# Performance work log

Hardware: AMD Instinct MI355X
Metric: run time of the kernel (lower is better)

The kernel has to match this reference:

```python
import jax, jax.numpy as jnp
import numpy as np

N_NODES = 50000
N_EDGES = 800000
N_GRAPHS = 8
BN_EPS = 1e-5


def setup_inputs() -> dict:
    key = jax.random.key(0)
    ks = iter(jax.random.split(key, 40))
    d = {}
    d["x"] = jax.random.normal(next(ks), (N_NODES, 3), dtype=jnp.float32)
    d["edge_index"] = jax.random.randint(next(ks), (2, N_EDGES), 0, N_NODES, dtype=jnp.int32)
    d["batch"] = jnp.sort(jax.random.randint(next(ks), (N_NODES,), 0, N_GRAPHS, dtype=jnp.int32))
    conv_in = [3, 64, 128]  # dense concat widths feeding each GCN layer
    for i, cin in enumerate(conv_in):
        d[f"W{i}"] = jax.random.normal(next(ks), (cin, 64), dtype=jnp.float32) * (1.0 / np.sqrt(cin))
        d[f"b{i}"] = jax.random.normal(next(ks), (64,), dtype=jnp.float32) * 0.05
        d[f"g{i}"] = jax.random.uniform(next(ks), (64,), dtype=jnp.float32) + 0.5
        d[f"beta{i}"] = jax.random.normal(next(ks), (64,), dtype=jnp.float32) * 0.05
        d[f"rm{i}"] = jax.random.normal(next(ks), (64,), dtype=jnp.float32) * 0.05
        d[f"rv{i}"] = jax.random.uniform(next(ks), (64,), dtype=jnp.float32) + 0.5
    def lin(k, i, o):
        return (jax.random.normal(k, (i, o), dtype=jnp.float32) * (1.0 / np.sqrt(i)),)
    d["enc_w0"], = lin(next(ks), 256, 128); d["enc_b0"] = jax.random.normal(next(ks), (128,), jnp.float32) * 0.05
    d["enc_w1"], = lin(next(ks), 128, 64); d["enc_b1"] = jax.random.normal(next(ks), (64,), jnp.float32) * 0.05
    d["dec_w0"], = lin(next(ks), 64, 32); d["dec_b0"] = jax.random.normal(next(ks), (32,), jnp.float32) * 0.05
    d["dec_w1"], = lin(next(ks), 32, 1); d["dec_b1"] = jax.random.normal(next(ks), (1,), jnp.float32) * 0.05
    return d


def reference(x, edge_index, batch,
              W0, b0, g0, beta0, rm0, rv0,
              W1, b1, g1, beta1, rm1, rv1,
              W2, b2, g2, beta2, rm2, rv2,
              enc_w0, enc_b0, enc_w1, enc_b1,
              dec_w0, dec_b0, dec_w1, dec_b1):
    N = x.shape[0]
    loops = jnp.arange(N, dtype=edge_index.dtype)
    src = jnp.concatenate([edge_index[0], loops])  # GCNConv adds self loops
    dst = jnp.concatenate([edge_index[1], loops])
    deg = jax.ops.segment_sum(jnp.ones_like(src, dtype=x.dtype), dst, num_segments=N)
    dinv = jnp.where(deg > 0, jax.lax.rsqrt(deg), 0.0)
    coef = (dinv[src] * dinv[dst])[:, None]  # symmetric normalization per edge

    def conv_bn_relu(h, W, b, g, beta, rm, rv):
        hw = h @ W                                    # [N, 64]
        out = jax.ops.segment_sum(hw[src] * coef, dst, num_segments=N) + b
        out = (out - rm) * (g * jax.lax.rsqrt(rv + BN_EPS)) + beta  # BN eval mode
        return jax.nn.relu(out)

    params = [(W0, b0, g0, beta0, rm0, rv0),
              (W1, b1, g1, beta1, rm1, rv1),
              (W2, b2, g2, beta2, rm2, rv2)]
    prev = []
    h = x
    for p in params:  # dense connectivity: concat all previous concat-outputs
        h = conv_bn_relu(h, *p)
        h = jnp.concatenate(prev + [h], axis=1)
        prev.append(h)

    e = jax.nn.relu(jax.nn.relu(h @ enc_w0 + enc_b0) @ enc_w1 + enc_b1)  # [N, 64]
    counts = jax.ops.segment_sum(jnp.ones((N,), x.dtype), batch, num_segments=N_GRAPHS)
    gfeat = jax.ops.segment_sum(e, batch, num_segments=N_GRAPHS) / jnp.maximum(counts, 1.0)[:, None]
    out = jax.nn.relu(gfeat @ dec_w0 + dec_b0) @ dec_w1 + dec_b1  # [G, 1]
    return out[:, 0]  # torch.squeeze(output, 1) since num_classes == 1
```

## Files before the change

kernel.cpp:

```cpp
#include <hip/hip_runtime.h>

#define NN 50000
#define NE 800000
#define NG 8
#define BN_EPS 1e-5f
#define NBLK ((NN + 255) / 256)
#define POOL_BLOCKS 512
#define NPART 8

typedef __attribute__((ext_vector_type(8))) short bf16x8;
typedef __attribute__((ext_vector_type(4))) float f32x4;

static __device__ __forceinline__ unsigned short f2bf(float f) {
    unsigned int u = __float_as_uint(f);
    unsigned int r = (u + 0x7FFFu + ((u >> 16) & 1u)) >> 16;
    return (unsigned short)r;
}
static __device__ __forceinline__ float bf2f(unsigned short h) {
    return __uint_as_float((unsigned int)h << 16);
}


__global__ __launch_bounds__(256) void count_deg(const int* __restrict__ dst,
                                                 int* __restrict__ degi) {
    int e = blockIdx.x * 256 + threadIdx.x;
    if (e < NE) atomicAdd(&degi[dst[e]], 1);
}

__global__ __launch_bounds__(256) void compute_dinv_xs(const int* __restrict__ degi,
                                                       const float* __restrict__ x,
                                                       float* __restrict__ dinv,
                                                       float* __restrict__ xs) {
    int i = blockIdx.x * 256 + threadIdx.x;
    if (i < NN) {
        float di = rsqrtf((float)(degi[i] + 1));
        dinv[i] = di;
        xs[i * 3 + 0] = x[i * 3 + 0] * di;
        xs[i * 3 + 1] = x[i * 3 + 1] * di;
        xs[i * 3 + 2] = x[i * 3 + 2] * di;
    }
}

__global__ __launch_bounds__(256) void scan_partial(const int* __restrict__ degi,
                                                    int* __restrict__ rowptr,
                                                    int* __restrict__ bsum) {
    __shared__ int sh[256];
    const int tid = threadIdx.x;
    const int i = blockIdx.x * 256 + tid;
    int v = (i < NN) ? degi[i] : 0;
    sh[tid] = v;
    __syncthreads();
#pragma unroll
    for (int off = 1; off < 256; off <<= 1) {
        int t = (tid >= off) ? sh[tid - off] : 0;
        __syncthreads();
        sh[tid] += t;
        __syncthreads();
    }
    if (i < NN) rowptr[i] = sh[tid] - v;
    if (tid == 255) bsum[blockIdx.x] = sh[255];
}

__global__ __launch_bounds__(256) void scan_bsums(int* __restrict__ bsum) {
    __shared__ int sh[256];
    const int tid = threadIdx.x;
    int v = (tid < NBLK) ? bsum[tid] : 0;
    sh[tid] = v;
    __syncthreads();
#pragma unroll
    for (int off = 1; off < 256; off <<= 1) {
        int t = (tid >= off) ? sh[tid - off] : 0;
        __syncthreads();
        sh[tid] += t;
        __syncthreads();
    }
    if (tid < NBLK) bsum[tid] = sh[tid] - v;
}

__global__ __launch_bounds__(256) void scan_finalize(const int* __restrict__ bsum,
                                                     int* __restrict__ rowptr,
                                                     int* __restrict__ cursor) {
    const int i = blockIdx.x * 256 + threadIdx.x;
    if (i < NN) {
        int r = rowptr[i] + bsum[blockIdx.x];
        rowptr[i] = r;
        cursor[i] = r;
    }
    if (i == 0) rowptr[NN] = NE;
}

__global__ __launch_bounds__(256) void fill_csr(const int* __restrict__ src,
                                                const int* __restrict__ dst,
                                                int* __restrict__ cursor,
                                                unsigned short* __restrict__ esrc16) {
    int e = blockIdx.x * 256 + threadIdx.x;
    if (e < NE) {
        int s = src[e], d = dst[e];
        int p = atomicAdd(&cursor[d], 1);
        esrc16[p] = (unsigned short)s;
    }
}


__global__ __launch_bounds__(256) void pack_w(const float* __restrict__ W, int K, int NOUT,
                                              unsigned short* __restrict__ ph,
                                              unsigned short* __restrict__ pl) {
    int idx = blockIdx.x * 256 + threadIdx.x;
    if (idx >= K * NOUT) return;
    int j = idx & 7;
    int lane = (idx >> 3) & 63;
    int rest = idx >> 9;
    int NF = NOUT >> 4;
    int f = rest % NF, ks = rest / NF;
    int k = ks * 32 + (lane >> 4) * 8 + j;
    int col = f * 16 + (lane & 15);
    float v = W[k * NOUT + col];
    unsigned short hi = f2bf(v);
    ph[idx] = hi;
    pl[idx] = f2bf(v - bf2f(hi));
}


template<int K, int NF, int MODE>
__global__ __launch_bounds__(256) void mfma_gemm(
        const unsigned short* __restrict__ Ahi,
        const unsigned short* __restrict__ Alo, int lda,
        const unsigned short* __restrict__ Bph,
        const unsigned short* __restrict__ Bpl,
        const float* __restrict__ bias,
        const float* __restrict__ dinv,
        float* __restrict__ outF,
        unsigned short* __restrict__ outHi,
        unsigned short* __restrict__ outLo, int ldo) {
    const int wave = threadIdx.x >> 6;
    const int lane = threadIdx.x & 63;
    const int rbase = blockIdx.x * 64 + wave * 16;
    int arow = rbase + (lane & 15);
    if (arow >= NN) arow = NN - 1;
    const int kbase = (lane >> 4) * 8;

    f32x4 acc[NF];
#pragma unroll
    for (int f = 0; f < NF; f++) acc[f] = (f32x4){0.f, 0.f, 0.f, 0.f};

    const unsigned short* pa_hi = Ahi + (size_t)arow * lda + kbase;
    const unsigned short* pa_lo = Alo + (size_t)arow * lda + kbase;
    const unsigned short* pb_hi = Bph + lane * 8;
    const unsigned short* pb_lo = Bpl + lane * 8;

#pragma unroll
    for (int ks = 0; ks < K / 32; ks++) {
        bf16x8 ah = *reinterpret_cast<const bf16x8*>(pa_hi + ks * 32);
        bf16x8 al = *reinterpret_cast<const bf16x8*>(pa_lo + ks * 32);
#pragma unroll
        for (int f = 0; f < NF; f++) {
            bf16x8 bh = *reinterpret_cast<const bf16x8*>(pb_hi + (size_t)((ks * NF + f) * 64) * 8);
            bf16x8 bl = *reinterpret_cast<const bf16x8*>(pb_lo + (size_t)((ks * NF + f) * 64) * 8);
            acc[f] = __builtin_amdgcn_mfma_f32_16x16x32_bf16(ah, bh, acc[f], 0, 0, 0);
            acc[f] = __builtin_amdgcn_mfma_f32_16x16x32_bf16(ah, bl, acc[f], 0, 0, 0);
            acc[f] = __builtin_amdgcn_mfma_f32_16x16x32_bf16(al, bh, acc[f], 0, 0, 0);
        }
    }

    const int drow0 = rbase + (lane >> 4) * 4;
    const int dcol = lane & 15;
#pragma unroll
    for (int f = 0; f < NF; f++) {
#pragma unroll
        for (int r = 0; r < 4; r++) {
            int row = drow0 + r;
            if (row < NN) {
                int col = f * 16 + dcol;
                float v = acc[f][r];
                if (MODE == 0) {
                    outF[(size_t)row * ldo + col] = v * dinv[row];
                } else {
                    v = fmaxf(v + bias[col], 0.0f);
                    if (MODE == 1) {
                        unsigned short hi = f2bf(v);
                        outHi[(size_t)row * ldo + col] = hi;
                        outLo[(size_t)row * ldo + col] = f2bf(v - bf2f(hi));
                    } else {
                        outF[(size_t)row * ldo + col] = v;
                    }
                }
            }
        }
    }
}


__global__ __launch_bounds__(256) void agg_x3(
        const float* __restrict__ xs,
        const int* __restrict__ rowptr,
        const unsigned short* __restrict__ esrc16,
        const float* __restrict__ dinv,
        float* __restrict__ ax) {
    const int i = blockIdx.x * 256 + threadIdx.x;
    if (i >= NN) return;
    float a0 = xs[i * 3 + 0];
    float a1 = xs[i * 3 + 1];
    float a2 = xs[i * 3 + 2];
    const int beg = rowptr[i], end = rowptr[i + 1];
    int e = beg;
    for (; e + 3 < end; e += 4) {
        int s0 = esrc16[e], s1 = esrc16[e + 1], s2 = esrc16[e + 2], s3 = esrc16[e + 3];
        a0 += xs[s0 * 3 + 0] + xs[s1 * 3 + 0] + xs[s2 * 3 + 0] + xs[s3 * 3 + 0];
        a1 += xs[s0 * 3 + 1] + xs[s1 * 3 + 1] + xs[s2 * 3 + 1] + xs[s3 * 3 + 1];
        a2 += xs[s0 * 3 + 2] + xs[s1 * 3 + 2] + xs[s2 * 3 + 2] + xs[s3 * 3 + 2];
    }
    for (; e < end; e++) {
        int s = esrc16[e];
        a0 += xs[s * 3 + 0];
        a1 += xs[s * 3 + 1];
        a2 += xs[s * 3 + 2];
    }
    const float di = dinv[i];
    ax[i * 3 + 0] = a0 * di;
    ax[i * 3 + 1] = a1 * di;
    ax[i * 3 + 2] = a2 * di;
}


__global__ __launch_bounds__(256) void l0_bn_relu(
        const float* __restrict__ ax, const float* __restrict__ W0,
        const float* __restrict__ b, const float* __restrict__ g,
        const float* __restrict__ beta, const float* __restrict__ rm,
        const float* __restrict__ rv,
        unsigned short* __restrict__ Hhi, unsigned short* __restrict__ Hlo) {
    const int t = blockIdx.x * 256 + threadIdx.x;
    const int row = t >> 6;
    const int ch = t & 63;
    if (row >= NN) return;
    float a0 = ax[row * 3 + 0], a1 = ax[row * 3 + 1], a2 = ax[row * 3 + 2];
    float v = a0 * W0[0 * 64 + ch] + a1 * W0[1 * 64 + ch] + a2 * W0[2 * 64 + ch] + b[ch];
    float sc = g[ch] * rsqrtf(rv[ch] + BN_EPS);
    v = (v - rm[ch]) * sc + beta[ch];
    v = fmaxf(v, 0.0f);
    unsigned short hi = f2bf(v);
    unsigned short lo = f2bf(v - bf2f(hi));
    Hhi[row * 256 + ch] = hi;
    Hlo[row * 256 + ch] = lo;
    Hhi[row * 256 + 64 + ch] = hi;
    Hlo[row * 256 + 64 + ch] = lo;
}


__global__ __launch_bounds__(256) void gather_bn_relu(
        const float* __restrict__ hws,
        const int* __restrict__ rowptr,
        const unsigned short* __restrict__ esrc16,
        const float* __restrict__ dinv,
        const float* __restrict__ b, const float* __restrict__ g,
        const float* __restrict__ beta, const float* __restrict__ rm,
        const float* __restrict__ rv,
        unsigned short* __restrict__ Hhi, unsigned short* __restrict__ Hlo) {
    const int wid = (blockIdx.x * 256 + threadIdx.x) >> 6;
    const int ch = threadIdx.x & 63;
    if (wid >= NN) return;
    const int beg = rowptr[wid], end = rowptr[wid + 1];
    float acc = hws[wid * 64 + ch];
    int e = beg;
    for (; e + 7 < end; e += 8) {
        int s0 = esrc16[e],     s1 = esrc16[e + 1], s2 = esrc16[e + 2], s3 = esrc16[e + 3];
        int s4 = esrc16[e + 4], s5 = esrc16[e + 5], s6 = esrc16[e + 6], s7 = esrc16[e + 7];
        float v0 = hws[s0 * 64 + ch], v1 = hws[s1 * 64 + ch];
        float v2 = hws[s2 * 64 + ch], v3 = hws[s3 * 64 + ch];
        float v4 = hws[s4 * 64 + ch], v5 = hws[s5 * 64 + ch];
        float v6 = hws[s6 * 64 + ch], v7 = hws[s7 * 64 + ch];
        acc += ((v0 + v1) + (v2 + v3)) + ((v4 + v5) + (v6 + v7));
    }
    for (; e < end; e++) acc += hws[esrc16[e] * 64 + ch];
    acc *= dinv[wid];
    float sc = g[ch] * rsqrtf(rv[ch] + BN_EPS);
    float v = (acc + b[ch] - rm[ch]) * sc + beta[ch];
    v = fmaxf(v, 0.0f);
    unsigned short hi = f2bf(v);
    unsigned short lo = f2bf(v - bf2f(hi));
    Hhi[wid * 256 + ch] = hi;
    Hlo[wid * 256 + ch] = lo;
}


__global__ __launch_bounds__(256) void pool_kernel(
        const float* __restrict__ e, const int* __restrict__ batch,
        float* __restrict__ gfeat_part, float* __restrict__ counts_part) {
    __shared__ float sh[4][NG][64];
    __shared__ float shc[4][NG];
    const int tid = threadIdx.x;
    const int ch = tid & 63;
    const int rg = tid >> 6;
    float acc[NG];
    float cnt[NG];
#pragma unroll
    for (int g = 0; g < NG; g++) { acc[g] = 0.0f; cnt[g] = 0.0f; }
    for (int i = blockIdx.x * 4 + rg; i < NN; i += POOL_BLOCKS * 4) {
        int b = batch[i];
        float v = e[i * 64 + ch];
#pragma unroll
        for (int g = 0; g < NG; g++) {
            acc[g] += (b == g) ? v : 0.0f;
            cnt[g] += (b == g) ? 1.0f : 0.0f;
        }
    }
#pragma unroll
    for (int g = 0; g < NG; g++) sh[rg][g][ch] = acc[g];
    if (ch == 0) {
#pragma unroll
        for (int g = 0; g < NG; g++) shc[rg][g] = cnt[g];
    }
    __syncthreads();
    const int p = blockIdx.x & (NPART - 1);
    if (rg == 0) {
#pragma unroll
        for (int g = 0; g < NG; g++) {
            float s = sh[0][g][ch] + sh[1][g][ch] + sh[2][g][ch] + sh[3][g][ch];
            atomicAdd(&gfeat_part[(p * NG + g) * 64 + ch], s);
        }
    }
    if (tid < NG) {
        float s = shc[0][tid] + shc[1][tid] + shc[2][tid] + shc[3][tid];
        atomicAdd(&counts_part[p * NG + tid], s);
    }
}


__global__ __launch_bounds__(256) void dec_kernel(
        const float* __restrict__ gfeat_part, const float* __restrict__ counts_part,
        const float* __restrict__ w0, const float* __restrict__ b0,
        const float* __restrict__ w1, const float* __restrict__ b1,
        float* __restrict__ out) {
    __shared__ float mg[NG][64];
    __shared__ float mc[NG];
    __shared__ float t1[NG][32];
    const int tid = threadIdx.x;
    for (int idx = tid; idx < NG * 64; idx += 256) {
        float s = 0.0f;
#pragma unroll
        for (int p = 0; p < NPART; p++) s += gfeat_part[p * NG * 64 + idx];
        mg[idx >> 6][idx & 63] = s;
    }
    if (tid < NG) {
        float s = 0.0f;
#pragma unroll
        for (int p = 0; p < NPART; p++) s += counts_part[p * NG + tid];
        mc[tid] = s;
    }
    __syncthreads();
    const int g = tid >> 5, c = tid & 31;
    float inv = 1.0f / fmaxf(mc[g], 1.0f);
    float acc = b0[c];
    for (int k = 0; k < 64; k++)
        acc = fmaf(mg[g][k] * inv, w0[k * 32 + c], acc);
    t1[g][c] = fmaxf(acc, 0.0f);
    __syncthreads();
    if (tid < NG) {
        float o = b1[0];
        for (int c2 = 0; c2 < 32; c2++) o = fmaf(t1[tid][c2], w1[c2], o);
        out[tid] = o;
    }
}


extern "C" void kernel_launch(void* const* d_in, const int* in_sizes, int n_in,
                              void* d_out, int out_size, void* d_ws, size_t ws_size,
                              hipStream_t stream) {
    const float* x      = (const float*)d_in[0];
    const int*   ei     = (const int*)d_in[1];
    const int*   batch  = (const int*)d_in[2];
    const float* W0     = (const float*)d_in[3];
    const float* b0     = (const float*)d_in[4];
    const float* g0     = (const float*)d_in[5];
    const float* beta0  = (const float*)d_in[6];
    const float* rm0    = (const float*)d_in[7];
    const float* rv0    = (const float*)d_in[8];
    const float* W1     = (const float*)d_in[9];
    const float* b1     = (const float*)d_in[10];
    const float* g1     = (const float*)d_in[11];
    const float* beta1  = (const float*)d_in[12];
    const float* rm1    = (const float*)d_in[13];
    const float* rv1    = (const float*)d_in[14];
    const float* W2     = (const float*)d_in[15];
    const float* b2     = (const float*)d_in[16];
    const float* g2     = (const float*)d_in[17];
    const float* beta2  = (const float*)d_in[18];
    const float* rm2    = (const float*)d_in[19];
    const float* rv2    = (const float*)d_in[20];
    const float* enc_w0 = (const float*)d_in[21];
    const float* enc_b0 = (const float*)d_in[22];
    const float* enc_w1 = (const float*)d_in[23];
    const float* enc_b1 = (const float*)d_in[24];
    const float* dec_w0 = (const float*)d_in[25];
    const float* dec_b0 = (const float*)d_in[26];
    const float* dec_w1 = (const float*)d_in[27];
    const float* dec_b1 = (const float*)d_in[28];

    const int* esrc = ei;
    const int* edst = ei + NE;

    char* wsb = (char*)d_ws;
    unsigned short* Hhi = (unsigned short*)wsb;
    unsigned short* Hlo = Hhi + (size_t)NN * 256;
    char* U = (char*)(Hlo + (size_t)NN * 256);
    unsigned short* Thi = (unsigned short*)U;
    unsigned short* Tlo = Thi + (size_t)NN * 128;
    int*   degi   = (int*)U;
    int*   rowptr = degi + NN;
    int*   cursor = rowptr + NN + 1;
    unsigned short* esrc16 = (unsigned short*)(cursor + NN);
    float* hws    = (float*)(U + (size_t)NN * 128 * 2 * sizeof(unsigned short));
    float* dinv   = hws + (size_t)NN * 64;
    float* xs     = dinv + NN;
    float* ax     = xs + (size_t)NN * 3;
    float* gfeat_part  = ax + (size_t)NN * 3;
    float* counts_part = gfeat_part + NPART * NG * 64;
    int*   bsum   = (int*)(counts_part + NPART * NG);
    unsigned short* wp = (unsigned short*)(bsum + NBLK);
    unsigned short* Wp1h = wp;              unsigned short* Wp1l = Wp1h + 64 * 64;
    unsigned short* Wp2h = Wp1l + 64 * 64;  unsigned short* Wp2l = Wp2h + 128 * 64;
    unsigned short* We0h = Wp2l + 128 * 64; unsigned short* We0l = We0h + 256 * 128;
    unsigned short* We1h = We0l + 256 * 128;unsigned short* We1l = We1h + 128 * 64;

    hipMemsetAsync(gfeat_part, 0, (NPART * NG * 64 + NPART * NG) * sizeof(float), stream);
    hipMemsetAsync(degi, 0, NN * sizeof(int), stream);

    count_deg<<<(NE + 255) / 256, 256, 0, stream>>>(edst, degi);
    compute_dinv_xs<<<NBLK, 256, 0, stream>>>(degi, x, dinv, xs);
    scan_partial<<<NBLK, 256, 0, stream>>>(degi, rowptr, bsum);
    scan_bsums<<<1, 256, 0, stream>>>(bsum);
    scan_finalize<<<NBLK, 256, 0, stream>>>(bsum, rowptr, cursor);
    fill_csr<<<(NE + 255) / 256, 256, 0, stream>>>(esrc, edst, cursor, esrc16);

    pack_w<<<(64 * 64 + 255) / 256, 256, 0, stream>>>(W1, 64, 64, Wp1h, Wp1l);
    pack_w<<<(128 * 64 + 255) / 256, 256, 0, stream>>>(W2, 128, 64, Wp2h, Wp2l);
    pack_w<<<(256 * 128 + 255) / 256, 256, 0, stream>>>(enc_w0, 256, 128, We0h, We0l);
    pack_w<<<(128 * 64 + 255) / 256, 256, 0, stream>>>(enc_w1, 128, 64, We1h, We1l);

    const int GRID_MFMA = (NN + 63) / 64;
    const int GRID_GATH = (NN * 64 + 255) / 256;

    agg_x3<<<NBLK, 256, 0, stream>>>(xs, rowptr, esrc16, dinv, ax);
    l0_bn_relu<<<GRID_GATH, 256, 0, stream>>>(ax, W0, b0, g0, beta0, rm0, rv0, Hhi, Hlo);

    mfma_gemm<64, 4, 0><<<GRID_MFMA, 256, 0, stream>>>(Hhi, Hlo, 256, Wp1h, Wp1l,
                                                       nullptr, dinv, hws, nullptr, nullptr, 64);
    gather_bn_relu<<<GRID_GATH, 256, 0, stream>>>(hws, rowptr, esrc16, dinv,
                                                  b1, g1, beta1, rm1, rv1, Hhi + 128, Hlo + 128);

    mfma_gemm<128, 4, 0><<<GRID_MFMA, 256, 0, stream>>>(Hhi + 64, Hlo + 64, 256, Wp2h, Wp2l,
                                                        nullptr, dinv, hws, nullptr, nullptr, 64);
    gather_bn_relu<<<GRID_GATH, 256, 0, stream>>>(hws, rowptr, esrc16, dinv,
                                                  b2, g2, beta2, rm2, rv2, Hhi + 192, Hlo + 192);

    mfma_gemm<256, 8, 1><<<GRID_MFMA, 256, 0, stream>>>(Hhi, Hlo, 256, We0h, We0l,
                                                        enc_b0, nullptr, nullptr, Thi, Tlo, 128);
    mfma_gemm<128, 4, 2><<<GRID_MFMA, 256, 0, stream>>>(Thi, Tlo, 128, We1h, We1l,
                                                        enc_b1, nullptr, hws, nullptr, nullptr, 64);

    pool_kernel<<<POOL_BLOCKS, 256, 0, stream>>>(hws, batch, gfeat_part, counts_part);
    dec_kernel<<<1, 256, 0, stream>>>(gfeat_part, counts_part, dec_w0, dec_b0, dec_w1, dec_b1, (float*)d_out);
}
```

Baseline: 279.8 us.

## Split gather into channel quarters and fold duplicated H block into encoder weight

```diff
diff --git a/kernel.cpp b/kernel.cpp
--- a/kernel.cpp
+++ b/kernel.cpp
@@ -7,6 +7,7 @@
 #define NBLK ((NN + 255) / 256)
 #define POOL_BLOCKS 512
 #define NPART 8
+#define HLD 192
 
 typedef __attribute__((ext_vector_type(8))) short bf16x8;
 typedef __attribute__((ext_vector_type(4))) float f32x4;
@@ -115,6 +116,26 @@
     int k = ks * 32 + (lane >> 4) * 8 + j;
     int col = f * 16 + (lane & 15);
     float v = W[k * NOUT + col];
+    unsigned short hi = f2bf(v);
+    ph[idx] = hi;
+    pl[idx] = f2bf(v - bf2f(hi));
+}
+
+__global__ __launch_bounds__(256) void pack_we0(const float* __restrict__ W,
+                                                unsigned short* __restrict__ ph,
+                                                unsigned short* __restrict__ pl) {
+    const int K = 192, NOUT = 128;
+    int idx = blockIdx.x * 256 + threadIdx.x;
+    if (idx >= K * NOUT) return;
+    int j = idx & 7;
+    int lane = (idx >> 3) & 63;
+    int rest = idx >> 9;
+    int NF = NOUT >> 4;
+    int f = rest % NF, ks = rest / NF;
+    int k = ks * 32 + (lane >> 4) * 8 + j;
+    int col = f * 16 + (lane & 15);
+    float v = (k < 64) ? (W[k * NOUT + col] + W[(k + 64) * NOUT + col])
+                       : W[(k + 64) * NOUT + col];
     unsigned short hi = f2bf(v);
     ph[idx] = hi;
     pl[idx] = f2bf(v - bf2f(hi));
@@ -170,11 +191,11 @@
         for (int r = 0; r < 4; r++) {
             int row = drow0 + r;
             if (row < NN) {
-                int col = f * 16 + dcol;
                 float v = acc[f][r];
                 if (MODE == 0) {
-                    outF[(size_t)row * ldo + col] = v * dinv[row];
+                    outF[((size_t)f * NN + row) * 16 + dcol] = v * dinv[row];
                 } else {
+                    int col = f * 16 + dcol;
                     v = fmaxf(v + bias[col], 0.0f);
                     if (MODE == 1) {
                         unsigned short hi = f2bf(v);
@@ -238,47 +259,51 @@
     v = (v - rm[ch]) * sc + beta[ch];
     v = fmaxf(v, 0.0f);
     unsigned short hi = f2bf(v);
-    unsigned short lo = f2bf(v - bf2f(hi));
-    Hhi[row * 256 + ch] = hi;
-    Hlo[row * 256 + ch] = lo;
-    Hhi[row * 256 + 64 + ch] = hi;
-    Hlo[row * 256 + 64 + ch] = lo;
-}
-
-
-__global__ __launch_bounds__(256) void gather_bn_relu(
-        const float* __restrict__ hws,
+    Hhi[(size_t)row * HLD + ch] = hi;
+    Hlo[(size_t)row * HLD + ch] = f2bf(v - bf2f(hi));
+}
+
+
+__global__ __launch_bounds__(256) void gather_bn_relu_q(
+        const float* __restrict__ hws4,
         const int* __restrict__ rowptr,
         const unsigned short* __restrict__ esrc16,
         const float* __restrict__ dinv,
         const float* __restrict__ b, const float* __restrict__ g,
         const float* __restrict__ beta, const float* __restrict__ rm,
         const float* __restrict__ rv,
-        unsigned short* __restrict__ Hhi, unsigned short* __restrict__ Hlo) {
-    const int wid = (blockIdx.x * 256 + threadIdx.x) >> 6;
-    const int ch = threadIdx.x & 63;
-    if (wid >= NN) return;
+        unsigned short* __restrict__ Hhi, unsigned short* __restrict__ Hlo, int cbase) {
+    const int BPQ = NN / 4;
+    const int q = blockIdx.x / BPQ;
+    const int bin = blockIdx.x - q * BPQ;
+    const int wave = threadIdx.x >> 6;
+    const int lane = threadIdx.x & 63;
+    const int wid = bin * 4 + wave;
+    const int ch = lane & 15;
+    const int grp = lane >> 4;
+    const float* __restrict__ tab = hws4 + (size_t)q * NN * 16;
     const int beg = rowptr[wid], end = rowptr[wid + 1];
-    float acc = hws[wid * 64 + ch];
-    int e = beg;
-    for (; e + 7 < end; e += 8) {
-        int s0 = esrc16[e],     s1 = esrc16[e + 1], s2 = esrc16[e + 2], s3 = esrc16[e + 3];
-        int s4 = esrc16[e + 4], s5 = esrc16[e + 5], s6 = esrc16[e + 6], s7 = esrc16[e + 7];
-        float v0 = hws[s0 * 64 + ch], v1 = hws[s1 * 64 + ch];
-        float v2 = hws[s2 * 64 + ch], v3 = hws[s3 * 64 + ch];
-        float v4 = hws[s4 * 64 + ch], v5 = hws[s5 * 64 + ch];
-        float v6 = hws[s6 * 64 + ch], v7 = hws[s7 * 64 + ch];
-        acc += ((v0 + v1) + (v2 + v3)) + ((v4 + v5) + (v6 + v7));
-    }
-    for (; e < end; e++) acc += hws[esrc16[e] * 64 + ch];
+    float acc = 0.0f;
+    int e = beg + grp;
+    for (; e + 4 < end; e += 8) {
+        int s0 = esrc16[e];
+        int s1 = esrc16[e + 4];
+        acc += tab[s0 * 16 + ch] + tab[s1 * 16 + ch];
+    }
+    if (e < end) acc += tab[esrc16[e] * 16 + ch];
+    acc += __shfl_xor(acc, 16, 64);
+    acc += __shfl_xor(acc, 32, 64);
+    acc += tab[wid * 16 + ch];
     acc *= dinv[wid];
-    float sc = g[ch] * rsqrtf(rv[ch] + BN_EPS);
-    float v = (acc + b[ch] - rm[ch]) * sc + beta[ch];
+    const int co = q * 16 + ch;
+    float sc = g[co] * rsqrtf(rv[co] + BN_EPS);
+    float v = (acc + b[co] - rm[co]) * sc + beta[co];
     v = fmaxf(v, 0.0f);
-    unsigned short hi = f2bf(v);
-    unsigned short lo = f2bf(v - bf2f(hi));
-    Hhi[wid * 256 + ch] = hi;
-    Hlo[wid * 256 + ch] = lo;
+    if (grp == 0) {
+        unsigned short hi = f2bf(v);
+        Hhi[(size_t)wid * HLD + cbase + co] = hi;
+        Hlo[(size_t)wid * HLD + cbase + co] = f2bf(v - bf2f(hi));
+    }
 }
 
 
@@ -400,8 +425,8 @@
 
     char* wsb = (char*)d_ws;
     unsigned short* Hhi = (unsigned short*)wsb;
-    unsigned short* Hlo = Hhi + (size_t)NN * 256;
-    char* U = (char*)(Hlo + (size_t)NN * 256);
+    unsigned short* Hlo = Hhi + (size_t)NN * HLD;
+    char* U = (char*)(Hlo + (size_t)NN * HLD);
     unsigned short* Thi = (unsigned short*)U;
     unsigned short* Tlo = Thi + (size_t)NN * 128;
     int*   degi   = (int*)U;
@@ -418,8 +443,8 @@
     unsigned short* wp = (unsigned short*)(bsum + NBLK);
     unsigned short* Wp1h = wp;              unsigned short* Wp1l = Wp1h + 64 * 64;
     unsigned short* Wp2h = Wp1l + 64 * 64;  unsigned short* Wp2l = Wp2h + 128 * 64;
-    unsigned short* We0h = Wp2l + 128 * 64; unsigned short* We0l = We0h + 256 * 128;
-    unsigned short* We1h = We0l + 256 * 128;unsigned short* We1l = We1h + 128 * 64;
+    unsigned short* We0h = Wp2l + 128 * 64; unsigned short* We0l = We0h + 192 * 128;
+    unsigned short* We1h = We0l + 192 * 128;unsigned short* We1l = We1h + 128 * 64;
 
     hipMemsetAsync(gfeat_part, 0, (NPART * NG * 64 + NPART * NG) * sizeof(float), stream);
     hipMemsetAsync(degi, 0, NN * sizeof(int), stream);
@@ -433,26 +458,27 @@
 
     pack_w<<<(64 * 64 + 255) / 256, 256, 0, stream>>>(W1, 64, 64, Wp1h, Wp1l);
     pack_w<<<(128 * 64 + 255) / 256, 256, 0, stream>>>(W2, 128, 64, Wp2h, Wp2l);
-    pack_w<<<(256 * 128 + 255) / 256, 256, 0, stream>>>(enc_w0, 256, 128, We0h, We0l);
+    pack_we0<<<(192 * 128 + 255) / 256, 256, 0, stream>>>(enc_w0, We0h, We0l);
     pack_w<<<(128 * 64 + 255) / 256, 256, 0, stream>>>(enc_w1, 128, 64, We1h, We1l);
 
     const int GRID_MFMA = (NN + 63) / 64;
-    const int GRID_GATH = (NN * 64 + 255) / 256;
+    const int GRID_L0   = (NN * 64 + 255) / 256;
+    const int GRID_GQ   = NN;
 
     agg_x3<<<NBLK, 256, 0, stream>>>(xs, rowptr, esrc16, dinv, ax);
-    l0_bn_relu<<<GRID_GATH, 256, 0, stream>>>(ax, W0, b0, g0, beta0, rm0, rv0, Hhi, Hlo);
-
-    mfma_gemm<64, 4, 0><<<GRID_MFMA, 256, 0, stream>>>(Hhi, Hlo, 256, Wp1h, Wp1l,
-                                                       nullptr, dinv, hws, nullptr, nullptr, 64);
-    gather_bn_relu<<<GRID_GATH, 256, 0, stream>>>(hws, rowptr, esrc16, dinv,
-                                                  b1, g1, beta1, rm1, rv1, Hhi + 128, Hlo + 128);
-
-    mfma_gemm<128, 4, 0><<<GRID_MFMA, 256, 0, stream>>>(Hhi + 64, Hlo + 64, 256, Wp2h, Wp2l,
-                                                        nullptr, dinv, hws, nullptr, nullptr, 64);
-    gather_bn_relu<<<GRID_GATH, 256, 0, stream>>>(hws, rowptr, esrc16, dinv,
-                                                  b2, g2, beta2, rm2, rv2, Hhi + 192, Hlo + 192);
-
-    mfma_gemm<256, 8, 1><<<GRID_MFMA, 256, 0, stream>>>(Hhi, Hlo, 256, We0h, We0l,
+    l0_bn_relu<<<GRID_L0, 256, 0, stream>>>(ax, W0, b0, g0, beta0, rm0, rv0, Hhi, Hlo);
+
+    mfma_gemm<64, 4, 0><<<GRID_MFMA, 256, 0, stream>>>(Hhi, Hlo, HLD, Wp1h, Wp1l,
+                                                       nullptr, dinv, hws, nullptr, nullptr, 0);
+    gather_bn_relu_q<<<GRID_GQ, 256, 0, stream>>>(hws, rowptr, esrc16, dinv,
+                                                  b1, g1, beta1, rm1, rv1, Hhi, Hlo, 64);
+
+    mfma_gemm<128, 4, 0><<<GRID_MFMA, 256, 0, stream>>>(Hhi, Hlo, HLD, Wp2h, Wp2l,
+                                                        nullptr, dinv, hws, nullptr, nullptr, 0);
+    gather_bn_relu_q<<<GRID_GQ, 256, 0, stream>>>(hws, rowptr, esrc16, dinv,
+                                                  b2, g2, beta2, rm2, rv2, Hhi, Hlo, 128);
+
+    mfma_gemm<192, 8, 1><<<GRID_MFMA, 256, 0, stream>>>(Hhi, Hlo, HLD, We0h, We0l,
                                                         enc_b0, nullptr, nullptr, Thi, Tlo, 128);
     mfma_gemm<128, 4, 2><<<GRID_MFMA, 256, 0, stream>>>(Thi, Tlo, 128, We1h, We1l,
                                                         enc_b1, nullptr, hws, nullptr, nullptr, 64);
```

Result: slower. 356.1 us (+27.3%).
